# Optimization experiments

Hardware: AMD Instinct MI355X
Metric: run time of the kernel (lower is better)

The kernel has to match this reference:

```python
import jax, jax.numpy as jnp
import numpy as np

B, L, H = 2, 512, 128

def setup_inputs() -> dict:
    key = jax.random.key(0)
    k1, k2, k3, _ = jax.random.split(key, 4)
    x = jax.random.normal(k1, (B, L, H), jnp.float32)
    y = jax.random.normal(k2, (B, L, H), jnp.float32)
    W_weight = jax.random.normal(k3, (H, 3 * H), jnp.float32) / np.sqrt(3 * H).astype(np.float32)
    W_bias = jnp.zeros((H,), jnp.float32)
    return {"x": x, "y": y, "W_weight": W_weight, "W_bias": W_bias}

def _span_max_context(x):
    """context[b,i,j,h] = max_{k=min(i,j)..max(i,j)} x[b,k,h], shape [B,L,L,H].
    Equivalent to the torch loop of diagonal running-max + symmetric scatter."""
    Bb, Ll, Hh = x.shape
    neg = jnp.full((Bb, 1, Hh), -jnp.inf, x.dtype)
    x_pad = jnp.concatenate([x, neg], axis=1)              # [B,L+1,H]
    d = jnp.arange(Ll)[:, None]                            # diagonal offset
    j = jnp.arange(Ll)[None, :]                            # start position
    shift_idx = jnp.minimum(d + j, Ll)                     # [L,L]; L -> -inf pad
    X2 = x_pad[:, shift_idx, :]                            # X2[b,d,j] = x[b,j+d]
    D = jax.lax.cummax(X2, axis=1)                         # D[b,d,j] = max_{k=j..j+d} x[b,k]
    i = jnp.arange(Ll)[:, None]
    jj = jnp.arange(Ll)[None, :]
    off = jnp.abs(i - jj)                                  # |i-j|
    lo = jnp.minimum(i, jj)                                # min(i,j)
    return D[:, off, lo, :]                                # [B,L,L,H]

def reference(x, y, W_weight, W_bias):
    Hh = x.shape[-1]
    ctx = _span_max_context(x)
    # Split W over the concat [x_i, y_j, context_ij] to avoid a [B,L,L,3H] intermediate.
    Wx, Wy, Wc = W_weight[:, :Hh], W_weight[:, Hh:2 * Hh], W_weight[:, 2 * Hh:]
    t = (jnp.einsum('blh,gh->blg', x, Wx)[:, :, None, :]
         + jnp.einsum('blh,gh->blg', y, Wy)[:, None, :, :]
         + jnp.einsum('bijh,gh->bijg', ctx, Wc)
         + W_bias)
    return jax.nn.gelu(t, approximate=False)               # [B,L,L,H]
```

## Files before the change

### kernel.cpp

```cpp
#include <hip/hip_runtime.h>
#include <hip/hip_bf16.h>

#define LL 512
#define HH 128
#define NBATCH 2
#define NT 32
#define NOFF (NT*(NT-1)/2)

typedef float f32x4 __attribute__((ext_vector_type(4)));
typedef short s16x8 __attribute__((ext_vector_type(8)));
typedef unsigned int u32x4 __attribute__((ext_vector_type(4)));

__device__ __forceinline__ unsigned short f2bfu(float f){
  __hip_bfloat16 h = __float2bfloat16(f);
  return __builtin_bit_cast(unsigned short, h);
}
__device__ __forceinline__ unsigned int bmax2(unsigned int a, unsigned int b){
  float lo = fmaxf(__uint_as_float(a << 16), __uint_as_float(b << 16));
  float hi = fmaxf(__uint_as_float(a & 0xFFFF0000u), __uint_as_float(b & 0xFFFF0000u));
  return __float_as_uint(hi) | (__float_as_uint(lo) >> 16);
}
__device__ __forceinline__ unsigned int fold3(unsigned int p, float gl, float gh,
                                              float g2l, float g2h){
  float lo = fmaxf(fmaxf(__uint_as_float(p << 16), gl), g2l);
  float hi = fmaxf(fmaxf(__uint_as_float(p & 0xFFFF0000u), gh), g2h);
  unsigned int lor = (__float_as_uint(lo) + 0x8000u) >> 16;
  unsigned int hir = (__float_as_uint(hi) + 0x8000u) & 0xFFFF0000u;
  return hir | lor;
}
__device__ __forceinline__ float gelu_f(float v){
  float inner = v * fmaf(0.044715f, v*v, 1.0f);
  float e = __expf(1.5957691216f * inner);
  float s = __fdividef(1.0f, e + 1.0f);
  return fmaf(-v, s, v);
}
__device__ __forceinline__ f32x4 gelu4(f32x4 v){
  f32x4 r;
  #pragma unroll
  for (int i=0;i<4;++i) r[i] = gelu_f(v[i]);
  return r;
}

__global__ void prep_kernel(const float* __restrict__ x, const float* __restrict__ y,
                            const float* __restrict__ W, const float* __restrict__ bias,
                            float* __restrict__ t1, float* __restrict__ t2,
                            float* __restrict__ bmax, short* __restrict__ Wcb){
  int blk = blockIdx.x, tid = threadIdx.x;
  if (blk < NBATCH*LL){
    int b = blk >> 9, l = blk & (LL-1);
    __shared__ float xs[HH], ys[HH];
    size_t base = ((size_t)b*LL + l)*HH;
    xs[tid] = x[base + tid];
    ys[tid] = y[base + tid];
    __syncthreads();
    const float4* wr1 = (const float4*)(W + (size_t)tid*384);
    const float4* wr2 = (const float4*)(W + (size_t)tid*384 + 128);
    const float4* xs4 = (const float4*)xs;
    const float4* ys4 = (const float4*)ys;
    float s1 = 0.f, s2 = 0.f;
    #pragma unroll
    for (int q=0;q<32;++q){
      float4 a = xs4[q], w = wr1[q];
      s1 = fmaf(a.x,w.x, fmaf(a.y,w.y, fmaf(a.z,w.z, fmaf(a.w,w.w, s1))));
      float4 c = ys4[q], w2 = wr2[q];
      s2 = fmaf(c.x,w2.x, fmaf(c.y,w2.y, fmaf(c.z,w2.z, fmaf(c.w,w2.w, s2))));
    }
    t1[base + tid] = s1 + bias[tid];
    t2[base + tid] = s2;
  } else if (blk < NBATCH*LL + NBATCH*NT){
    int e = blk - NBATCH*LL;
    int b = e >> 5, t = e & 31;
    float m = -INFINITY;
    #pragma unroll
    for (int r=0;r<16;++r) m = fmaxf(m, x[((size_t)b*LL + t*16 + r)*HH + tid]);
    bmax[(size_t)e*HH + tid] = m;
  } else {
    int g = blk - (NBATCH*LL + NBATCH*NT);
    Wcb[g*HH + tid] = (short)f2bfu(W[(size_t)g*384 + 256 + tid]);
  }
}

__global__ __launch_bounds__(512, 4) void ctx_kernel(
    const float* __restrict__ x, const float* __restrict__ t1,
    const float* __restrict__ t2, const float* __restrict__ bmax,
    const short* __restrict__ Wcb, float* __restrict__ out)
{
  __shared__ __align__(16) unsigned int shbuf[5*16*64];
  const int tid = threadIdx.x;
  const int b = blockIdx.y;
  const int w = tid >> 6, l = tid & 63, l16 = l & 15, lhi = l >> 4;
  const int g0 = w*16 + lhi*4;

  s16x8 wcf[4];
  #pragma unroll
  for (int kb=0;kb<4;++kb)
    wcf[kb] = *(const s16x8*)(Wcb + (size_t)(w*16 + l16)*HH + kb*32 + lhi*8);

  if (blockIdx.x < NOFF) {
    int ti = 0, tj;
    { int rem = blockIdx.x;
      while (rem >= NT-1-ti){ rem -= NT-1-ti; ++ti; }
      tj = ti + 1 + rem; }

    unsigned short* sfxU = (unsigned short*)shbuf;
    unsigned short* pfxU = (unsigned short*)(shbuf + 1024);
    float* gmaxS = (float*)(shbuf + 2048);

    {
      int role = tid >> 7, h = tid & 127;
      if (role == 0){
        const float* xp = x + ((size_t)b*LL + ti*16)*HH + h;
        float v[16];
        #pragma unroll
        for (int r=0;r<16;++r) v[r] = xp[(size_t)r*HH];
        float run = -INFINITY;
        #pragma unroll
        for (int r=15;r>=0;--r){ run = fmaxf(run, v[r]);
          sfxU[r*HH + (h ^ ((r&7)<<3))] = f2bfu(run); }
      } else if (role == 1){
        const float* xp = x + ((size_t)b*LL + tj*16)*HH + h;
        float v[16];
        #pragma unroll
        for (int r=0;r<16;++r) v[r] = xp[(size_t)r*HH];
        float run = -INFINITY;
        #pragma unroll
        for (int r=0;r<16;++r){ run = fmaxf(run, v[r]);
          pfxU[r*HH + (h ^ ((r&7)<<3))] = f2bfu(run); }
      } else {
        int half = role - 2;
        float g = -INFINITY;
        for (int t = ti+1+half; t < tj; t += 2)
          g = fmaxf(g, bmax[((size_t)b*NT + t)*HH + h]);
        gmaxS[half*HH + h] = g;
      }
    }
    __syncthreads();

    unsigned int pfxg[16];
    const unsigned int* pfxW = shbuf + 1024;
    #pragma unroll
    for (int kb=0;kb<4;++kb){
      int h0 = kb*32 + lhi*8;
      int wd0 = (h0 >> 1) ^ ((l16&7)<<2);
      u32x4 u = *(const u32x4*)&pfxW[l16*64 + wd0];
      float4 ga = *(const float4*)&gmaxS[h0];
      float4 gb = *(const float4*)&gmaxS[h0+4];
      float4 gc = *(const float4*)&gmaxS[HH + h0];
      float4 gd = *(const float4*)&gmaxS[HH + h0+4];
      pfxg[kb*4+0] = fold3(u[0], ga.x, ga.y, gc.x, gc.y);
      pfxg[kb*4+1] = fold3(u[1], ga.z, ga.w, gc.z, gc.w);
      pfxg[kb*4+2] = fold3(u[2], gb.x, gb.y, gd.x, gd.y);
      pfxg[kb*4+3] = fold3(u[3], gb.z, gb.w, gd.z, gd.w);
    }

    const size_t qoff = ((size_t)b*LL + tj*16 + l16)*HH + g0;
    f32x4 t1j = *(const f32x4*)(t1 + qoff);
    f32x4 t2j = *(const f32x4*)(t2 + qoff);
    const float* t1ip = t1 + ((size_t)b*LL + ti*16)*HH + g0;
    const float* t2ip = t2 + ((size_t)b*LL + ti*16)*HH + g0;
    float* o1base = out + (((size_t)(b*LL + ti*16))*LL + tj*16 + l16)*HH + g0;
    float* o2base = out + (((size_t)(b*LL + tj*16 + l16))*LL + ti*16)*HH + g0;
    const unsigned int* sfxW = shbuf;

    #pragma unroll
    for (int pt=0; pt<16; ++pt){
      f32x4 acc = (f32x4){0.f,0.f,0.f,0.f};
      #pragma unroll
      for (int kb=0;kb<4;++kb){
        int wd0 = ((kb*32 + lhi*8) >> 1) ^ ((pt&7)<<2);
        u32x4 s = *(const u32x4*)&sfxW[pt*64 + wd0];
        unsigned int f0 = bmax2(s[0], pfxg[kb*4+0]);
        unsigned int f1 = bmax2(s[1], pfxg[kb*4+1]);
        unsigned int f2 = bmax2(s[2], pfxg[kb*4+2]);
        unsigned int f3 = bmax2(s[3], pfxg[kb*4+3]);
        u32x4 fr = (u32x4){f0,f1,f2,f3};
        acc = __builtin_amdgcn_mfma_f32_16x16x32_bf16(wcf[kb],
                __builtin_bit_cast(s16x8, fr), acc, 0, 0, 0);
      }
      f32x4 t1i = *(const f32x4*)(t1ip + (size_t)pt*HH);
      f32x4 t2i = *(const f32x4*)(t2ip + (size_t)pt*HH);
      *(f32x4*)(o1base + (size_t)pt*LL*HH) = gelu4(acc + t1i + t2j);
      *(f32x4*)(o2base + (size_t)pt*HH)    = gelu4(acc + t1j + t2i);
    }
  } else {
    const int td = blockIdx.x - NOFF;
    #pragma unroll
    for (int it=0; it<2; ++it){
      int e = tid*2 + it;
      int r = e >> 6, wd = e & 63;
      float2 a = *(const float2*)(x + ((size_t)b*LL + td*16 + r)*HH + wd*2);
      unsigned int u = ((__float_as_uint(a.y) + 0x8000u) & 0xFFFF0000u)
                     | ((__float_as_uint(a.x) + 0x8000u) >> 16);
      shbuf[(0*16 + r)*64 + (wd ^ ((r&7)<<2))] = u;
    }
    __syncthreads();
    #pragma unroll
    for (int k=1;k<5;++k){
      int step = 1 << (k-1);
      unsigned int res[2]; int dst[2];
      #pragma unroll
      for (int it=0; it<2; ++it){
        int e = tid*2 + it;
        int r = e >> 6, wd = e & 63;
        int r2 = min(r + step, 15);
        unsigned int a = shbuf[((k-1)*16 + r )*64 + (wd ^ ((r &7)<<2))];
        unsigned int c = shbuf[((k-1)*16 + r2)*64 + (wd ^ ((r2&7)<<2))];
        res[it] = bmax2(a, c);
        dst[it] = (k*16 + r)*64 + (wd ^ ((r&7)<<2));
      }
      shbuf[dst[0]] = res[0];
      shbuf[dst[1]] = res[1];
      __syncthreads();
    }

    const size_t qoff = ((size_t)b*LL + td*16 + l16)*HH + g0;
    f32x4 t2j = *(const f32x4*)(t2 + qoff);
    const float* t1ip = t1 + ((size_t)b*LL + td*16)*HH + g0;
    float* obase = out + (((size_t)(b*LL + td*16))*LL + td*16 + l16)*HH + g0;

    #pragma unroll
    for (int pt=0; pt<16; ++pt){
      int a  = min(pt, l16), bb = max(pt, l16);
      int len = bb - a + 1;
      int k = 31 - __clz(len);
      int r2 = bb + 1 - (1 << k);
      f32x4 acc = (f32x4){0.f,0.f,0.f,0.f};
      #pragma unroll
      for (int kb=0;kb<4;++kb){
        int wd0 = (kb*32 + lhi*8) >> 1;
        u32x4 ua = *(const u32x4*)&shbuf[(k*16 + a )*64 + ((wd0) ^ ((a &7)<<2))];
        u32x4 ub = *(const u32x4*)&shbuf[(k*16 + r2)*64 + ((wd0) ^ ((r2&7)<<2))];
        unsigned int f0 = bmax2(ua[0], ub[0]);
        unsigned int f1 = bmax2(ua[1], ub[1]);
        unsigned int f2 = bmax2(ua[2], ub[2]);
        unsigned int f3 = bmax2(ua[3], ub[3]);
        u32x4 fr = (u32x4){f0,f1,f2,f3};
        acc = __builtin_amdgcn_mfma_f32_16x16x32_bf16(wcf[kb],
                __builtin_bit_cast(s16x8, fr), acc, 0, 0, 0);
      }
      f32x4 t1i = *(const f32x4*)(t1ip + (size_t)pt*HH);
      *(f32x4*)(obase + (size_t)pt*LL*HH) = gelu4(acc + t1i + t2j);
    }
  }
}

extern "C" void kernel_launch(void* const* d_in, const int* in_sizes, int n_in,
                              void* d_out, int out_size, void* d_ws, size_t ws_size,
                              hipStream_t stream) {
  const float* x    = (const float*)d_in[0];
  const float* y    = (const float*)d_in[1];
  const float* W    = (const float*)d_in[2];
  const float* bias = (const float*)d_in[3];
  float* out = (float*)d_out;

  float* t1 = (float*)d_ws;
  float* t2 = t1 + (size_t)NBATCH*LL*HH;
  float* bmax = t2 + (size_t)NBATCH*LL*HH;
  short* Wcb = (short*)(bmax + (size_t)NBATCH*NT*HH);

  prep_kernel<<<NBATCH*LL + NBATCH*NT + HH, HH, 0, stream>>>(x, y, W, bias, t1, t2, bmax, Wcb);
  ctx_kernel<<<dim3(NOFF + NT, NBATCH), 512, 0, stream>>>(x, t1, t2, bmax, Wcb, out);
}
```

Measured before the change: 109.6 us.

## Halve ctx block size, reassign waves to row pairs over all output channels

The context kernel drops from 512 to 256 threads per block. Each wave now owns four row positions and loops over all eight 16-channel output tiles, reloading the bf16 Wc fragments from global memory per tile instead of holding one channel slice in registers. Two MFMA chains are interleaved per tile. The gmax fold now happens while building the prefix in shared memory, and the diagonal sparse table shrinks to four levels. The prep kernel is widened to 256 threads, splitting x/y projections across thread halves. This trades more Wcb reloads and per-wave serial work for smaller LDS and register footprint, aiming for higher occupancy and fewer shared-memory conversions.

After: 100.6 us. -8.2%, faster.

```diff
diff --git a/kernel.cpp b/kernel.cpp
--- a/kernel.cpp
+++ b/kernel.cpp
@@ -20,13 +20,13 @@
   float hi = fmaxf(__uint_as_float(a & 0xFFFF0000u), __uint_as_float(b & 0xFFFF0000u));
   return __float_as_uint(hi) | (__float_as_uint(lo) >> 16);
 }
-__device__ __forceinline__ unsigned int fold3(unsigned int p, float gl, float gh,
-                                              float g2l, float g2h){
-  float lo = fmaxf(fmaxf(__uint_as_float(p << 16), gl), g2l);
-  float hi = fmaxf(fmaxf(__uint_as_float(p & 0xFFFF0000u), gh), g2h);
-  unsigned int lor = (__float_as_uint(lo) + 0x8000u) >> 16;
-  unsigned int hir = (__float_as_uint(hi) + 0x8000u) & 0xFFFF0000u;
-  return hir | lor;
+__device__ __forceinline__ unsigned int packbf2(float lo, float hi){
+  return ((__float_as_uint(hi) + 0x8000u) & 0xFFFF0000u)
+       | ((__float_as_uint(lo) + 0x8000u) >> 16);
+}
+__device__ __forceinline__ u32x4 bmax4(u32x4 a, u32x4 b){
+  u32x4 r; r[0]=bmax2(a[0],b[0]); r[1]=bmax2(a[1],b[1]);
+  r[2]=bmax2(a[2],b[2]); r[3]=bmax2(a[3],b[3]); return r;
 }
 __device__ __forceinline__ float gelu_f(float v){
   float inner = v * fmaf(0.044715f, v*v, 1.0f);
@@ -50,51 +50,51 @@
     int b = blk >> 9, l = blk & (LL-1);
     __shared__ float xs[HH], ys[HH];
     size_t base = ((size_t)b*LL + l)*HH;
-    xs[tid] = x[base + tid];
-    ys[tid] = y[base + tid];
+    if (tid < HH) xs[tid] = x[base + tid];
+    else          ys[tid-HH] = y[base + tid - HH];
     __syncthreads();
-    const float4* wr1 = (const float4*)(W + (size_t)tid*384);
-    const float4* wr2 = (const float4*)(W + (size_t)tid*384 + 128);
-    const float4* xs4 = (const float4*)xs;
-    const float4* ys4 = (const float4*)ys;
-    float s1 = 0.f, s2 = 0.f;
-    #pragma unroll
-    for (int q=0;q<32;++q){
-      float4 a = xs4[q], w = wr1[q];
-      s1 = fmaf(a.x,w.x, fmaf(a.y,w.y, fmaf(a.z,w.z, fmaf(a.w,w.w, s1))));
-      float4 c = ys4[q], w2 = wr2[q];
-      s2 = fmaf(c.x,w2.x, fmaf(c.y,w2.y, fmaf(c.z,w2.z, fmaf(c.w,w2.w, s2))));
-    }
-    t1[base + tid] = s1 + bias[tid];
-    t2[base + tid] = s2;
-  } else if (blk < NBATCH*LL + NBATCH*NT){
-    int e = blk - NBATCH*LL;
+    int role = tid >> 7, g = tid & (HH-1);
+    const float4* wr = (const float4*)(W + (size_t)g*384 + role*HH);
+    const float4* vs = (const float4*)(role ? ys : xs);
+    float sA = 0.f, sB = 0.f;
+    #pragma unroll
+    for (int q=0;q<32;q+=2){
+      float4 a = vs[q],   w1 = wr[q];
+      sA = fmaf(a.x,w1.x, fmaf(a.y,w1.y, fmaf(a.z,w1.z, fmaf(a.w,w1.w, sA))));
+      float4 c = vs[q+1], w2 = wr[q+1];
+      sB = fmaf(c.x,w2.x, fmaf(c.y,w2.y, fmaf(c.z,w2.z, fmaf(c.w,w2.w, sB))));
+    }
+    float s = sA + sB;
+    if (role == 0) t1[base + g] = s + bias[g];
+    else           t2[base + g] = s;
+  } else if (blk < NBATCH*LL + NBATCH*NT/2){
+    int e = (blk - NBATCH*LL)*2 + (tid >> 7);
+    int h = tid & (HH-1);
     int b = e >> 5, t = e & 31;
     float m = -INFINITY;
     #pragma unroll
-    for (int r=0;r<16;++r) m = fmaxf(m, x[((size_t)b*LL + t*16 + r)*HH + tid]);
-    bmax[(size_t)e*HH + tid] = m;
+    for (int r=0;r<16;++r) m = fmaxf(m, x[((size_t)b*LL + t*16 + r)*HH + h]);
+    bmax[(size_t)e*HH + h] = m;
   } else {
-    int g = blk - (NBATCH*LL + NBATCH*NT);
-    Wcb[g*HH + tid] = (short)f2bfu(W[(size_t)g*384 + 256 + tid]);
+    int e0 = ((blk - (NBATCH*LL + NBATCH*NT/2))*256 + tid)*8;
+    #pragma unroll
+    for (int i=0;i<8;++i){
+      int e = e0 + i; int g = e >> 7, h = e & (HH-1);
+      Wcb[e] = (short)f2bfu(W[(size_t)g*384 + 256 + h]);
+    }
   }
 }
 
-__global__ __launch_bounds__(512, 4) void ctx_kernel(
+__global__ __launch_bounds__(256, 4) void ctx_kernel(
     const float* __restrict__ x, const float* __restrict__ t1,
     const float* __restrict__ t2, const float* __restrict__ bmax,
     const short* __restrict__ Wcb, float* __restrict__ out)
 {
-  __shared__ __align__(16) unsigned int shbuf[5*16*64];
+  __shared__ __align__(16) unsigned short shs[8192];
   const int tid = threadIdx.x;
   const int b = blockIdx.y;
   const int w = tid >> 6, l = tid & 63, l16 = l & 15, lhi = l >> 4;
-  const int g0 = w*16 + lhi*4;
-
-  s16x8 wcf[4];
-  #pragma unroll
-  for (int kb=0;kb<4;++kb)
-    wcf[kb] = *(const s16x8*)(Wcb + (size_t)(w*16 + l16)*HH + kb*32 + lhi*8);
+  const size_t bL = (size_t)b*LL;
 
   if (blockIdx.x < NOFF) {
     int ti = 0, tj;
@@ -102,144 +102,149 @@
       while (rem >= NT-1-ti){ rem -= NT-1-ti; ++ti; }
       tj = ti + 1 + rem; }
 
-    unsigned short* sfxU = (unsigned short*)shbuf;
-    unsigned short* pfxU = (unsigned short*)(shbuf + 1024);
-    float* gmaxS = (float*)(shbuf + 2048);
-
-    {
-      int role = tid >> 7, h = tid & 127;
+    unsigned short* sfxU = shs;
+    unsigned short* pfgU = shs + 2048;
+    { int role = tid >> 7, h = tid & (HH-1);
       if (role == 0){
-        const float* xp = x + ((size_t)b*LL + ti*16)*HH + h;
-        float v[16];
-        #pragma unroll
-        for (int r=0;r<16;++r) v[r] = xp[(size_t)r*HH];
+        const float* xp = x + (bL + ti*16)*HH + h;
         float run = -INFINITY;
         #pragma unroll
-        for (int r=15;r>=0;--r){ run = fmaxf(run, v[r]);
+        for (int r=15;r>=0;--r){ run = fmaxf(run, xp[r*HH]);
           sfxU[r*HH + (h ^ ((r&7)<<3))] = f2bfu(run); }
-      } else if (role == 1){
-        const float* xp = x + ((size_t)b*LL + tj*16)*HH + h;
-        float v[16];
-        #pragma unroll
-        for (int r=0;r<16;++r) v[r] = xp[(size_t)r*HH];
+      } else {
+        const float* bp = bmax + ((size_t)b*NT)*HH + h;
         float run = -INFINITY;
-        #pragma unroll
-        for (int r=0;r<16;++r){ run = fmaxf(run, v[r]);
-          pfxU[r*HH + (h ^ ((r&7)<<3))] = f2bfu(run); }
-      } else {
-        int half = role - 2;
-        float g = -INFINITY;
-        for (int t = ti+1+half; t < tj; t += 2)
-          g = fmaxf(g, bmax[((size_t)b*NT + t)*HH + h]);
-        gmaxS[half*HH + h] = g;
+        for (int t=ti+1; t<tj; ++t) run = fmaxf(run, bp[t*HH]);
+        const float* xp = x + (bL + tj*16)*HH + h;
+        #pragma unroll
+        for (int r=0;r<16;++r){ run = fmaxf(run, xp[r*HH]);
+          pfgU[r*HH + (h ^ ((r&7)<<3))] = f2bfu(run); }
       }
     }
     __syncthreads();
 
-    unsigned int pfxg[16];
-    const unsigned int* pfxW = shbuf + 1024;
-    #pragma unroll
-    for (int kb=0;kb<4;++kb){
-      int h0 = kb*32 + lhi*8;
-      int wd0 = (h0 >> 1) ^ ((l16&7)<<2);
-      u32x4 u = *(const u32x4*)&pfxW[l16*64 + wd0];
-      float4 ga = *(const float4*)&gmaxS[h0];
-      float4 gb = *(const float4*)&gmaxS[h0+4];
-      float4 gc = *(const float4*)&gmaxS[HH + h0];
-      float4 gd = *(const float4*)&gmaxS[HH + h0+4];
-      pfxg[kb*4+0] = fold3(u[0], ga.x, ga.y, gc.x, gc.y);
-      pfxg[kb*4+1] = fold3(u[1], ga.z, ga.w, gc.z, gc.w);
-      pfxg[kb*4+2] = fold3(u[2], gb.x, gb.y, gd.x, gd.y);
-      pfxg[kb*4+3] = fold3(u[3], gb.z, gb.w, gd.z, gd.w);
-    }
-
-    const size_t qoff = ((size_t)b*LL + tj*16 + l16)*HH + g0;
-    f32x4 t1j = *(const f32x4*)(t1 + qoff);
-    f32x4 t2j = *(const f32x4*)(t2 + qoff);
-    const float* t1ip = t1 + ((size_t)b*LL + ti*16)*HH + g0;
-    const float* t2ip = t2 + ((size_t)b*LL + ti*16)*HH + g0;
-    float* o1base = out + (((size_t)(b*LL + ti*16))*LL + tj*16 + l16)*HH + g0;
-    float* o2base = out + (((size_t)(b*LL + tj*16 + l16))*LL + ti*16)*HH + g0;
-    const unsigned int* sfxW = shbuf;
-
-    #pragma unroll
-    for (int pt=0; pt<16; ++pt){
-      f32x4 acc = (f32x4){0.f,0.f,0.f,0.f};
+    const int qrow = tj*16 + l16;
+    const size_t qoff = (bL + qrow)*HH;
+
+    #pragma unroll
+    for (int ph=0; ph<2; ++ph){
+      const int pt0 = w*4 + ph*2, pt1 = pt0 + 1;
+      u32x4 fr0[4], fr1[4];
       #pragma unroll
       for (int kb=0;kb<4;++kb){
-        int wd0 = ((kb*32 + lhi*8) >> 1) ^ ((pt&7)<<2);
-        u32x4 s = *(const u32x4*)&sfxW[pt*64 + wd0];
-        unsigned int f0 = bmax2(s[0], pfxg[kb*4+0]);
-        unsigned int f1 = bmax2(s[1], pfxg[kb*4+1]);
-        unsigned int f2 = bmax2(s[2], pfxg[kb*4+2]);
-        unsigned int f3 = bmax2(s[3], pfxg[kb*4+3]);
-        u32x4 fr = (u32x4){f0,f1,f2,f3};
-        acc = __builtin_amdgcn_mfma_f32_16x16x32_bf16(wcf[kb],
-                __builtin_bit_cast(s16x8, fr), acc, 0, 0, 0);
-      }
-      f32x4 t1i = *(const f32x4*)(t1ip + (size_t)pt*HH);
-      f32x4 t2i = *(const f32x4*)(t2ip + (size_t)pt*HH);
-      *(f32x4*)(o1base + (size_t)pt*LL*HH) = gelu4(acc + t1i + t2j);
-      *(f32x4*)(o2base + (size_t)pt*HH)    = gelu4(acc + t1j + t2i);
+        int h0 = kb*32 + lhi*8;
+        u32x4 p  = *(const u32x4*)&pfgU[l16*HH + (h0 ^ ((l16&7)<<3))];
+        u32x4 s0 = *(const u32x4*)&sfxU[pt0*HH + (h0 ^ ((pt0&7)<<3))];
+        u32x4 s1 = *(const u32x4*)&sfxU[pt1*HH + (h0 ^ ((pt1&7)<<3))];
+        fr0[kb] = bmax4(s0, p);
+        fr1[kb] = bmax4(s1, p);
+      }
+      const size_t i0off = (bL + ti*16 + pt0)*HH;
+      const size_t i1off = (bL + ti*16 + pt1)*HH;
+      const size_t o1r0 = ((bL + ti*16 + pt0)*LL + qrow)*HH;
+      const size_t o1r1 = ((bL + ti*16 + pt1)*LL + qrow)*HH;
+      const size_t o2r0 = ((bL + qrow)*LL + ti*16 + pt0)*HH;
+      const size_t o2r1 = o2r0 + HH;
+
+      #pragma unroll
+      for (int nt=0; nt<8; ++nt){
+        const int gg = nt*16 + l16;
+        s16x8 wcf[4];
+        #pragma unroll
+        for (int kb=0;kb<4;++kb)
+          wcf[kb] = *(const s16x8*)(Wcb + (size_t)gg*HH + kb*32 + lhi*8);
+        f32x4 a0 = (f32x4){0.f,0.f,0.f,0.f}, a1 = a0;
+        #pragma unroll
+        for (int kb=0;kb<4;++kb){
+          a0 = __builtin_amdgcn_mfma_f32_16x16x32_bf16(wcf[kb],
+                 __builtin_bit_cast(s16x8, fr0[kb]), a0, 0, 0, 0);
+          a1 = __builtin_amdgcn_mfma_f32_16x16x32_bf16(wcf[kb],
+                 __builtin_bit_cast(s16x8, fr1[kb]), a1, 0, 0, 0);
+        }
+        const int g0 = nt*16 + lhi*4;
+        f32x4 t1j = *(const f32x4*)(t1 + qoff + g0);
+        f32x4 t2j = *(const f32x4*)(t2 + qoff + g0);
+        f32x4 t1i0 = *(const f32x4*)(t1 + i0off + g0);
+        f32x4 t2i0 = *(const f32x4*)(t2 + i0off + g0);
+        f32x4 t1i1 = *(const f32x4*)(t1 + i1off + g0);
+        f32x4 t2i1 = *(const f32x4*)(t2 + i1off + g0);
+        *(f32x4*)(out + o1r0 + g0) = gelu4(a0 + t1i0 + t2j);
+        *(f32x4*)(out + o2r0 + g0) = gelu4(a0 + t1j + t2i0);
+        *(f32x4*)(out + o1r1 + g0) = gelu4(a1 + t1i1 + t2j);
+        *(f32x4*)(out + o2r1 + g0) = gelu4(a1 + t1j + t2i1);
+      }
     }
   } else {
     const int td = blockIdx.x - NOFF;
-    #pragma unroll
-    for (int it=0; it<2; ++it){
-      int e = tid*2 + it;
-      int r = e >> 6, wd = e & 63;
-      float2 a = *(const float2*)(x + ((size_t)b*LL + td*16 + r)*HH + wd*2);
-      unsigned int u = ((__float_as_uint(a.y) + 0x8000u) & 0xFFFF0000u)
-                     | ((__float_as_uint(a.x) + 0x8000u) >> 16);
-      shbuf[(0*16 + r)*64 + (wd ^ ((r&7)<<2))] = u;
+    unsigned short* M = shs;
+    { int e = tid*8; int r = e >> 7, h0 = e & (HH-1);
+      const float* xp = x + (bL + td*16 + r)*HH + h0;
+      f32x4 v0 = *(const f32x4*)xp, v1 = *(const f32x4*)(xp+4);
+      u32x4 pk; pk[0]=packbf2(v0[0],v0[1]); pk[1]=packbf2(v0[2],v0[3]);
+      pk[2]=packbf2(v1[0],v1[1]); pk[3]=packbf2(v1[2],v1[3]);
+      *(u32x4*)&M[r*HH + (h0 ^ ((r&7)<<3))] = pk;
     }
     __syncthreads();
     #pragma unroll
-    for (int k=1;k<5;++k){
-      int step = 1 << (k-1);
-      unsigned int res[2]; int dst[2];
-      #pragma unroll
-      for (int it=0; it<2; ++it){
-        int e = tid*2 + it;
-        int r = e >> 6, wd = e & 63;
-        int r2 = min(r + step, 15);
-        unsigned int a = shbuf[((k-1)*16 + r )*64 + (wd ^ ((r &7)<<2))];
-        unsigned int c = shbuf[((k-1)*16 + r2)*64 + (wd ^ ((r2&7)<<2))];
-        res[it] = bmax2(a, c);
-        dst[it] = (k*16 + r)*64 + (wd ^ ((r&7)<<2));
-      }
-      shbuf[dst[0]] = res[0];
-      shbuf[dst[1]] = res[1];
+    for (int k=1;k<4;++k){
+      int e = tid*8; int r = e >> 7, h0 = e & (HH-1);
+      int r2 = min(r + (1<<(k-1)), 15);
+      u32x4 a = *(const u32x4*)&M[((k-1)*16 + r )*HH + (h0 ^ ((r &7)<<3))];
+      u32x4 c = *(const u32x4*)&M[((k-1)*16 + r2)*HH + (h0 ^ ((r2&7)<<3))];
+      *(u32x4*)&M[(k*16 + r)*HH + (h0 ^ ((r&7)<<3))] = bmax4(a, c);
       __syncthreads();
     }
 
-    const size_t qoff = ((size_t)b*LL + td*16 + l16)*HH + g0;
-    f32x4 t2j = *(const f32x4*)(t2 + qoff);
-    const float* t1ip = t1 + ((size_t)b*LL + td*16)*HH + g0;
-    float* obase = out + (((size_t)(b*LL + td*16))*LL + td*16 + l16)*HH + g0;
-
-    #pragma unroll
-    for (int pt=0; pt<16; ++pt){
-      int a  = min(pt, l16), bb = max(pt, l16);
-      int len = bb - a + 1;
-      int k = 31 - __clz(len);
-      int r2 = bb + 1 - (1 << k);
-      f32x4 acc = (f32x4){0.f,0.f,0.f,0.f};
-      #pragma unroll
-      for (int kb=0;kb<4;++kb){
-        int wd0 = (kb*32 + lhi*8) >> 1;
-        u32x4 ua = *(const u32x4*)&shbuf[(k*16 + a )*64 + ((wd0) ^ ((a &7)<<2))];
-        u32x4 ub = *(const u32x4*)&shbuf[(k*16 + r2)*64 + ((wd0) ^ ((r2&7)<<2))];
-        unsigned int f0 = bmax2(ua[0], ub[0]);
-        unsigned int f1 = bmax2(ua[1], ub[1]);
-        unsigned int f2 = bmax2(ua[2], ub[2]);
-        unsigned int f3 = bmax2(ua[3], ub[3]);
-        u32x4 fr = (u32x4){f0,f1,f2,f3};
-        acc = __builtin_amdgcn_mfma_f32_16x16x32_bf16(wcf[kb],
-                __builtin_bit_cast(s16x8, fr), acc, 0, 0, 0);
-      }
-      f32x4 t1i = *(const f32x4*)(t1ip + (size_t)pt*HH);
-      *(f32x4*)(obase + (size_t)pt*LL*HH) = gelu4(acc + t1i + t2j);
+    const int qrow = td*16 + l16;
+    const size_t qoff = (bL + qrow)*HH;
+
+    #pragma unroll
+    for (int ph=0; ph<2; ++ph){
+      const int ptA = w*4 + ph*2;
+      u32x4 fr[2][4];
+      #pragma unroll
+      for (int pi=0; pi<2; ++pi){
+        int pt = ptA + pi;
+        int a = min(pt, l16), bb = max(pt, l16);
+        int len = bb - a + 1;
+        int k = 31 - __clz(len); if (k > 3) k = 3;
+        int r2 = bb + 1 - (1 << k);
+        #pragma unroll
+        for (int kb=0;kb<4;++kb){
+          int h0 = kb*32 + lhi*8;
+          u32x4 ua = *(const u32x4*)&M[(k*16 + a )*HH + (h0 ^ ((a &7)<<3))];
+          u32x4 ub = *(const u32x4*)&M[(k*16 + r2)*HH + (h0 ^ ((r2&7)<<3))];
+          fr[pi][kb] = bmax4(ua, ub);
+        }
+      }
+      const int pt0 = ptA, pt1 = ptA + 1;
+      const size_t i0off = (bL + td*16 + pt0)*HH;
+      const size_t i1off = (bL + td*16 + pt1)*HH;
+      const size_t o0 = ((bL + td*16 + pt0)*LL + qrow)*HH;
+      const size_t o1 = ((bL + td*16 + pt1)*LL + qrow)*HH;
+
+      #pragma unroll
+      for (int nt=0; nt<8; ++nt){
+        const int gg = nt*16 + l16;
+        s16x8 wcf[4];
+        #pragma unroll
+        for (int kb=0;kb<4;++kb)
+          wcf[kb] = *(const s16x8*)(Wcb + (size_t)gg*HH + kb*32 + lhi*8);
+        f32x4 a0 = (f32x4){0.f,0.f,0.f,0.f}, a1 = a0;
+        #pragma unroll
+        for (int kb=0;kb<4;++kb){
+          a0 = __builtin_amdgcn_mfma_f32_16x16x32_bf16(wcf[kb],
+                 __builtin_bit_cast(s16x8, fr[0][kb]), a0, 0, 0, 0);
+          a1 = __builtin_amdgcn_mfma_f32_16x16x32_bf16(wcf[kb],
+                 __builtin_bit_cast(s16x8, fr[1][kb]), a1, 0, 0, 0);
+        }
+        const int g0 = nt*16 + lhi*4;
+        f32x4 t2j = *(const f32x4*)(t2 + qoff + g0);
+        f32x4 t1i0 = *(const f32x4*)(t1 + i0off + g0);
+        f32x4 t1i1 = *(const f32x4*)(t1 + i1off + g0);
+        *(f32x4*)(out + o0 + g0) = gelu4(a0 + t1i0 + t2j);
+        *(f32x4*)(out + o1 + g0) = gelu4(a1 + t1i1 + t2j);
+      }
     }
   }
 }
@@ -258,6 +263,6 @@
   float* bmax = t2 + (size_t)NBATCH*LL*HH;
   short* Wcb = (short*)(bmax + (size_t)NBATCH*NT*HH);
 
-  prep_kernel<<<NBATCH*LL + NBATCH*NT + HH, HH, 0, stream>>>(x, y, W, bias, t1, t2, bmax, Wcb);
-  ctx_kernel<<<dim3(NOFF + NT, NBATCH), 512, 0, stream>>>(x, t1, t2, bmax, Wcb, out);
-}
+  prep_kernel<<<NBATCH*LL + NBATCH*NT/2 + 8, 256, 0, stream>>>(x, y, W, bias, t1, t2, bmax, Wcb);
+  ctx_kernel<<<dim3(NOFF + NT, NBATCH), 256, 0, stream>>>(x, t1, t2, bmax, Wcb, out);
+}
```
